# Performance work log

Measured on AMD Instinct MI355X. Metric: run time of the kernel, lower is better.

## Reference

```python
import math
import jax
import jax.numpy as jnp
import numpy as np

N_HE = 50000          # number of hyperedges (molecules)
E = 1200000           # edges per node type (incidence nnz)
IN_FEAT = 200
HE_DIM = 512
E_DIM = 128
Q_DIM = 64
V_DIM = 128
N_M, N_P, N_G = 167, 881, 441   # node counts (fingerprint bit vocabularies)
D_M, D_P, D_G = 167, 881, 441   # node feature dims
SCALE = 1.0 / math.sqrt(Q_DIM)


def _seg_attn(k, q, v, src, dst, n_dst):
    # per-edge score <k[src], q[dst]>/sqrt(q_dim) -> leaky_relu -> softmax over edges sharing dst -> weighted scatter-sum of v[src]
    att = jax.nn.leaky_relu(jnp.sum(k[src] * q[dst], axis=-1) * SCALE)
    m = jax.ops.segment_max(att, dst, num_segments=n_dst)
    m = jnp.where(jnp.isfinite(m), m, 0.0)  # guard empty segments
    ex = jnp.exp(att - m[dst])
    denom = jax.ops.segment_sum(ex, dst, num_segments=n_dst)
    agg = jax.ops.segment_sum(ex[:, None] * v[src], dst, num_segments=n_dst)
    return agg / jnp.maximum(denom, 1e-20)[:, None]


def setup_inputs() -> dict:
    key = jax.random.key(0)
    ks = iter(jax.random.split(key, 64))

    def nrm(shape, scale=1.0):
        return jax.random.normal(next(ks), shape, jnp.float32) * scale

    def lin(din, dout):
        return nrm((din, dout), 1.0 / math.sqrt(din)), jnp.zeros((dout,), jnp.float32)

    inp = {}
    inp["he_feat"] = nrm((N_HE, IN_FEAT))
    inp["maccs_feat"] = nrm((N_M, D_M))
    inp["pubchem_feat"] = nrm((N_P, D_P))
    inp["erg_feat"] = nrm((N_G, D_G))
    inp["w1_w"], inp["w1_b"] = lin(IN_FEAT, HE_DIM)
    inp["w2_w"], inp["w2_b"] = lin(HE_DIM, E_DIM)
    inp["w3_w"], inp["w3_b"] = lin(HE_DIM, Q_DIM)
    inp["w4_w"], inp["w4_b"] = lin(HE_DIM, V_DIM)
    inp["w5m_w"], inp["w5m_b"] = lin(D_M, Q_DIM)
    inp["w5p_w"], inp["w5p_b"] = lin(D_P, Q_DIM)
    inp["w5e_w"], inp["w5e_b"] = lin(D_G, Q_DIM)
    inp["w6m_w"], inp["w6m_b"] = lin(Q_DIM, E_DIM)
    inp["w7m_w"], inp["w7m_b"] = lin(Q_DIM, E_DIM)
    inp["w6p_w"], inp["w6p_b"] = lin(Q_DIM, E_DIM)
    inp["w7p_w"], inp["w7p_b"] = lin(Q_DIM, E_DIM)
    inp["w6e_w"], inp["w6e_b"] = lin(Q_DIM, E_DIM)
    inp["w7e_w"], inp["w7e_b"] = lin(Q_DIM, E_DIM)
    inp["mlp1_w"], inp["mlp1_b"] = lin(3 * E_DIM, 2 * E_DIM)
    inp["mlp2_w"], inp["mlp2_b"] = lin(2 * E_DIM, E_DIM)
    inp["src_maccs"] = jax.random.randint(next(ks), (E,), 0, N_HE, jnp.int32)
    inp["dst_maccs"] = jax.random.randint(next(ks), (E,), 0, N_M, jnp.int32)
    inp["src_pubchem"] = jax.random.randint(next(ks), (E,), 0, N_HE, jnp.int32)
    inp["dst_pubchem"] = jax.random.randint(next(ks), (E,), 0, N_P, jnp.int32)
    inp["src_erg"] = jax.random.randint(next(ks), (E,), 0, N_HE, jnp.int32)
    inp["dst_erg"] = jax.random.randint(next(ks), (E,), 0, N_G, jnp.int32)
    return inp


def reference(he_feat, maccs_feat, pubchem_feat, erg_feat,
              w1_w, w1_b, w2_w, w2_b, w3_w, w3_b, w4_w, w4_b,
              w5m_w, w5m_b, w5p_w, w5p_b, w5e_w, w5e_b,
              w6m_w, w6m_b, w7m_w, w7m_b,
              w6p_w, w6p_b, w7p_w, w7p_b,
              w6e_w, w6e_b, w7e_w, w7e_b,
              mlp1_w, mlp1_b, mlp2_w, mlp2_b,
              src_maccs, dst_maccs, src_pubchem, dst_pubchem, src_erg, dst_erg):
    n_he = he_feat.shape[0]
    e_feat = he_feat @ w1_w + w1_b            # [N_HE, he_dim] (w1, first_layer=True)
    k_he = e_feat @ w3_w + w3_b               # [N_HE, q_dim]
    v_he = e_feat @ w4_w + w4_b               # [N_HE, v_dim]
    q_from_nodes = e_feat @ w2_w + w2_b       # [N_HE, e_dim]
    groups = [
        (maccs_feat, w5m_w, w5m_b, w6m_w, w6m_b, w7m_w, w7m_b, src_maccs, dst_maccs),
        (pubchem_feat, w5p_w, w5p_b, w6p_w, w6p_b, w7p_w, w7p_b, src_pubchem, dst_pubchem),
        (erg_feat, w5e_w, w5e_b, w6e_w, w6e_b, w7e_w, w7e_b, src_erg, dst_erg),
    ]
    msgs = []
    for feat, w5w, w5b, w6w, w6b, w7w, w7b, src, dst in groups:
        q = feat @ w5w + w5b                  # node queries [N_t, q_dim]
        # hyperedge -> node attention (writes node 'feat'; not consumed by this forward's output, kept for fidelity)
        _node_feat_new = _seg_attn(k_he, q, v_he, src, dst, feat.shape[0])
        # node -> hyperedge attention (note: uses q, i.e. the pre-update node projection, as in the source)
        k2 = q @ w6w + w6b                    # [N_t, e_dim]
        v2 = q @ w7w + w7b                    # [N_t, e_dim]
        msgs.append(_seg_attn(k2, q_from_nodes, v2, dst, src, n_he))
    he_new = jnp.concatenate(msgs, axis=-1)   # [N_HE, 3*e_dim]
    x = jax.nn.relu(he_new @ mlp1_w + mlp1_b)  # dropout: eval mode -> identity
    x = jax.nn.relu(x @ mlp2_w + mlp2_b)
    return x                                   # [N_HE, e_dim] (last_layer=False, eval)
```

## Files before the change

kernel.cpp:

```cpp
#include <hip/hip_runtime.h>
#include <hip/hip_bf16.h>

typedef __hip_bfloat16 bf16;
typedef float f32x4 __attribute__((ext_vector_type(4)));
typedef short bf16x8s __attribute__((ext_vector_type(8)));
typedef unsigned short u16x8 __attribute__((ext_vector_type(8)));

constexpr int N_HE = 50000;
constexpr int M_PAD = 50048;
constexpr int E_EDGES = 1200000;
constexpr int IN_F = 200;
constexpr int KP_HE = 224;
constexpr int HE_DIM = 512;
constexpr int E_DIM = 128;
constexpr int Q_DIM = 64;
constexpr float SL2E = 0.125f * 1.44269504088896f;
constexpr int N_NODES = 1489;
constexpr int R_STRIDE = 216;
constexpr int T_STRIDE = 192;
constexpr int LDSD = 40;
constexpr int NBIN = 98;
constexpr int BIN_SHIFT = 9;
constexpr int ECHUNK = 4096;
constexpr int NCHUNK = (E_EDGES + ECHUNK - 1) / ECHUNK;
constexpr int BINCAP = 13056;
constexpr int SCAT_BLKS = 3 * NCHUNK;
constexpr int PREP_BLKS = 650 + N_NODES;

struct EdgeIdx { const int* p[3]; };

__device__ __forceinline__ void split2(float v, bf16& h, bf16& l)
{
    bf16 hb = __float2bfloat16(v);
    h = hb;
    l = __float2bfloat16(v - __bfloat162float(hb));
}
__device__ __forceinline__ void split2u(float v, unsigned short& h, unsigned short& l)
{
    bf16 hb = __float2bfloat16(v);
    bf16 lb = __float2bfloat16(v - __bfloat162float(hb));
    h = *reinterpret_cast<unsigned short*>(&hb);
    l = *reinterpret_cast<unsigned short*>(&lb);
}
__device__ __forceinline__ float exp2_fast(float x)
{
    float r;
    asm("v_exp_f32 %0, %1" : "=v"(r) : "v"(x));
    return r;
}
__device__ __forceinline__ float red16(float x)
{
    x += __int_as_float(__builtin_amdgcn_update_dpp(0, __float_as_int(x), 0xB1, 0xF, 0xF, true));
    x += __int_as_float(__builtin_amdgcn_update_dpp(0, __float_as_int(x), 0x4E, 0xF, 0xF, true));
    x += __int_as_float(__builtin_amdgcn_update_dpp(0, __float_as_int(x), 0x141, 0xF, 0xF, true));
    x += __int_as_float(__builtin_amdgcn_update_dpp(0, __float_as_int(x), 0x140, 0xF, 0xF, true));
    return x;
}

struct PrepArgs {
    const float *w1w, *w1b, *w2w, *w2b;
    float *W12f, *b12;
    const float *w6[3], *b6[3];
    float *Bkvf;
    const float *w7[3], *b7[3];
    const float *mlp1w, *mlp1b;
    bf16 *Wct_hi, *Wct_lo;
    float *b_comp;
    const float *mlp2w;
    bf16 *Wm2t_hi, *Wm2t_lo;
    const float *feat[3], *w5[3], *b5[3];
    float *q_t;
};

__global__ __launch_bounds__(256) void scatter_prep_fused_kernel(
    EdgeIdx S, EdgeIdx D, int* __restrict__ bincursor, unsigned* __restrict__ binbuf,
    PrepArgs P)
{
    __shared__ unsigned stage[ECHUNK];
    __shared__ int hist4[4][NBIN];
    __shared__ int hist[NBIN], off[NBIN], cur[NBIN], gbase[NBIN];
    int bid = blockIdx.x, tid = threadIdx.x;
    if (bid < SCAT_BLKS) {
        int g = bid / NCHUNK, chunk = bid - g * NCHUNK;
        const int* src = S.p[g];
        const int* dst = D.p[g];
        int lane = tid & 63, w = tid >> 6;
        for (int b = tid; b < 4 * NBIN; b += 256) (&hist4[0][0])[b] = 0;
        __syncthreads();
        int base = chunk * ECHUNK;
        int s[ECHUNK / 256], d[ECHUNK / 256];
#pragma unroll
        for (int k = 0; k < ECHUNK / 256; ++k) {
            int i = base + k * 256 + tid;
            if (i < E_EDGES) {
                s[k] = src[i];
                d[k] = dst[i];
                atomicAdd(&hist4[w][s[k] >> BIN_SHIFT], 1);
            } else s[k] = -1;
        }
        __syncthreads();
        if (w == 0) {
            int i1 = 64 + lane;
            int v0 = 0, v1 = 0;
            if (lane < NBIN) v0 = hist4[0][lane] + hist4[1][lane] + hist4[2][lane] + hist4[3][lane];
            if (i1 < NBIN) v1 = hist4[0][i1] + hist4[1][i1] + hist4[2][i1] + hist4[3][i1];
            int x0 = v0, x1 = v1;
#pragma unroll
            for (int o = 1; o < 64; o <<= 1) {
                int t0 = __shfl_up(x0, o, 64);
                int t1 = __shfl_up(x1, o, 64);
                if (lane >= o) { x0 += t0; x1 += t1; }
            }
            int tot0 = __shfl(x0, 63, 64);
            if (lane < NBIN) { hist[lane] = v0; off[lane] = x0 - v0; cur[lane] = x0 - v0; }
            if (i1 < NBIN) { hist[i1] = v1; off[i1] = tot0 + x1 - v1; cur[i1] = tot0 + x1 - v1; }
        }
        __syncthreads();
        if (tid < NBIN) gbase[tid] = hist[tid] ? atomicAdd(&bincursor[g * NBIN + tid], hist[tid]) : 0;
        __syncthreads();
#pragma unroll
        for (int k = 0; k < ECHUNK / 256; ++k) {
            if (s[k] >= 0) {
                int bin = s[k] >> BIN_SHIFT;
                int pos = atomicAdd(&cur[bin], 1);
                stage[pos] = ((unsigned)(s[k] & 511) << 10) | (unsigned)d[k];
            }
        }
        __syncthreads();
        size_t gslot = (size_t)g * NBIN * BINCAP;
        for (int b = w; b < NBIN; b += 4) {
            int len = hist[b];
            if (!len) continue;
            int gb = gbase[b];
            int avail = BINCAP - gb;
            if (avail <= 0) continue;
            if (len > avail) len = avail;
            int lo = off[b];
            size_t obase = gslot + (size_t)b * BINCAP + gb;
            for (int j = lane; j < len; j += 64)
                binbuf[obase + j] = stage[lo + j];
        }
        return;
    }
    float* sh = (float*)stage;
    int pb = bid - SCAT_BLKS;
    if (pb < 201) {
        int row = pb;
        int col = tid & 127, ks = tid >> 7;
        const float* a = (row < IN_F) ? (P.w1w + (size_t)row * HE_DIM) : P.w1b;
        float s = 0.f;
#pragma unroll 4
        for (int k = ks; k < HE_DIM; k += 2)
            s = fmaf(a[k], P.w2w[k * E_DIM + col], s);
        sh[ks * 128 + col] = s;
        __syncthreads();
        if (ks == 0) {
            float v = sh[col] + sh[128 + col];
            if (row < IN_F) P.W12f[row * E_DIM + col] = v;
            else P.b12[col] = v + P.w2b[col];
        }
    } else if (pb < 329) {
        int k = pb - 201;
        int c = tid;
        if (c < R_STRIDE) {
            int g = c / 72, j = c - g * 72;
            float v = 0.f;
            if (j < 64) v = P.w6[g][j * E_DIM + k];
            else if (j == 64) v = P.b6[g][k];
            P.Bkvf[k * R_STRIDE + c] = v;
        }
    } else if (pb < 522) {
        int row = pb - 329;
        int n = tid;
        if (row < 192) {
            int g = row >> 6, i = row & 63;
            const float* w7 = P.w7[g];
            float s = 0.f;
#pragma unroll 4
            for (int k = 0; k < 128; ++k)
                s = fmaf(w7[i * 128 + k], P.mlp1w[(size_t)(g * 128 + k) * 256 + n], s);
            bf16 h, l; split2(s, h, l);
            P.Wct_hi[n * T_STRIDE + row] = h;
            P.Wct_lo[n * T_STRIDE + row] = l;
        } else {
            float s = P.mlp1b[n];
            for (int g = 0; g < 3; ++g)
#pragma unroll 4
                for (int k = 0; k < 128; ++k)
                    s = fmaf(P.b7[g][k], P.mlp1w[(size_t)(g * 128 + k) * 256 + n], s);
            P.b_comp[n] = s;
        }
    } else if (pb < 650) {
        int n = pb - 522;
        int k = tid;
        float v = P.mlp2w[(size_t)k * 128 + n];
        bf16 h, l; split2(v, h, l);
        P.Wm2t_hi[n * 256 + k] = h;
        P.Wm2t_lo[n * 256 + k] = l;
    } else {
        int b = pb - 650;
        int g = (b < 167) ? 0 : (b < 1048 ? 1 : 2);
        int row = b - (g == 0 ? 0 : (g == 1 ? 167 : 1048));
        int Dt = (g == 0) ? 167 : (g == 1 ? 881 : 441);
        const float* feat = P.feat[g] + (size_t)row * Dt;
        const float* w5 = P.w5[g];
        int col = tid & 63, ks = tid >> 6;
        float s = 0.f;
#pragma unroll 4
        for (int k = ks; k < Dt; k += 4)
            s = fmaf(feat[k], w5[k * Q_DIM + col], s);
        sh[ks * 64 + col] = s;
        __syncthreads();
        if (ks == 0)
            P.q_t[(size_t)b * Q_DIM + col] =
                sh[col] + sh[64 + col] + sh[128 + col] + sh[192 + col] + P.b5[g][col];
    }
}

__global__ __launch_bounds__(256) void csr_wr_fused_kernel(
    const unsigned* __restrict__ binbuf, const int* __restrict__ bincursor,
    int2* __restrict__ rows2_all, int* __restrict__ ebuf,
    const float* __restrict__ W12f, const float* __restrict__ b12,
    const float* __restrict__ Bkvf,
    bf16* __restrict__ WRt_hi, bf16* __restrict__ WRt_lo, float* __restrict__ bR)
{
    __shared__ int hist[512], cur[512], cs[8];
    __shared__ float fcol[128];
    int bid = blockIdx.x, tid = threadIdx.x;
    if (bid < 3 * NBIN) {
        int g = bid / NBIN, b = bid - g * NBIN;
        int cnt = min(bincursor[g * NBIN + b], BINCAP);
        size_t sbase = ((size_t)g * NBIN + b) * BINCAP;
        int h0 = b << BIN_SHIFT;
        int hN = min(512, N_HE - h0);
        int ebase_rel = b * BINCAP;
        int2* rows2 = rows2_all + g * N_HE;
        int lane = tid & 63, w = tid >> 6;
        hist[tid] = 0; hist[tid + 256] = 0;
        __syncthreads();
        for (int i = tid; i < cnt; i += 256)
            atomicAdd(&hist[binbuf[sbase + i] >> 10], 1);
        __syncthreads();
#pragma unroll
        for (int c2 = 0; c2 < 2; ++c2) {
            int c = w * 2 + c2, idx = c * 64 + lane;
            int v = hist[idx], x = v;
#pragma unroll
            for (int o = 1; o < 64; o <<= 1) {
                int t = __shfl_up(x, o, 64);
                if (lane >= o) x += t;
            }
            cur[idx] = x - v;
            if (lane == 63) cs[c] = x;
        }
        __syncthreads();
        if (tid == 0) {
            int run = 0;
#pragma unroll
            for (int c = 0; c < 8; ++c) { int t = cs[c]; cs[c] = run; run += t; }
        }
        __syncthreads();
#pragma unroll
        for (int c2 = 0; c2 < 2; ++c2) {
            int c = w * 2 + c2, idx = c * 64 + lane;
            int e = cur[idx] + cs[c];
            cur[idx] = e;
            if (idx < hN) rows2[h0 + idx] = make_int2(ebase_rel + e, ebase_rel + e + hist[idx]);
        }
        __syncthreads();
        for (int i = tid; i < cnt; i += 256) {
            unsigned p = binbuf[sbase + i];
            int pos = atomicAdd(&cur[p >> 10], 1);
            ebuf[sbase + pos] = (int)((p & 1023u) << 8);
        }
    } else {
        int c = bid - 3 * NBIN;
        const bf16 z = __float2bfloat16(0.f);
        if (c >= R_STRIDE) {
            if (tid < KP_HE) { WRt_hi[c * KP_HE + tid] = z; WRt_lo[c * KP_HE + tid] = z; }
            return;
        }
        if (tid < 128) fcol[tid] = Bkvf[tid * R_STRIDE + c];
        __syncthreads();
        if (tid < IN_F) {
            const float* wrow = W12f + (size_t)tid * E_DIM;
            float s = 0.f;
#pragma unroll 4
            for (int k = 0; k < 128; ++k) s = fmaf(wrow[k], fcol[k], s);
            bf16 h, l; split2(s * SL2E, h, l);
            WRt_hi[c * KP_HE + tid] = h;
            WRt_lo[c * KP_HE + tid] = l;
        } else if (tid < KP_HE) {
            WRt_hi[c * KP_HE + tid] = z;
            WRt_lo[c * KP_HE + tid] = z;
        } else if (tid == KP_HE) {
            float s = 0.f;
            for (int k = 0; k < 128; ++k) s = fmaf(b12[k], fcol[k], s);
            bR[c] = s * SL2E;
        }
    }
}

template <bool GUARD, bool BIAS, bool RELU>
__global__ __launch_bounds__(256) void mfma_gemm_kernel(
    const float* __restrict__ A, int lda, int Kp, int Mvalid,
    const bf16* __restrict__ Bthg, const bf16* __restrict__ Btlg,
    const float* __restrict__ bias,
    float* __restrict__ C, int M, int N, int ldc)
{
    __shared__ bf16 Ah[128 * LDSD], Al[128 * LDSD], Bh[64 * LDSD], Bl[64 * LDSD];
    const int tid = threadIdx.x;
    const int bm = blockIdx.x * 128, bn = blockIdx.y * 64;
    const int lane = tid & 63, w = tid >> 6;
    const int kgrp = lane >> 4, lr = lane & 15;
    const int arow = tid >> 1, ahalf = (tid & 1) * 16;
    const int brow = tid >> 2, bq = (tid & 3) * 8;
    f32x4 acc[2][4] = {};

    for (int k0 = 0; k0 < Kp; k0 += 32) {
        {
            int row = bm + arow, kb = k0 + ahalf;
            float va[16];
            if (!GUARD || (row < Mvalid && kb + 16 <= lda)) {
                const float* ap = A + (size_t)row * lda + kb;
                *(float4*)&va[0]  = *(const float4*)ap;
                *(float4*)&va[4]  = *(const float4*)(ap + 4);
                *(float4*)&va[8]  = *(const float4*)(ap + 8);
                *(float4*)&va[12] = *(const float4*)(ap + 12);
            } else {
#pragma unroll
                for (int j = 0; j < 16; ++j) {
                    int k = kb + j;
                    va[j] = (row < Mvalid && k < lda) ? A[(size_t)row * lda + k] : 0.f;
                }
            }
            u16x8 H0, H1, L0, L1;
#pragma unroll
            for (int j = 0; j < 8; ++j) {
                unsigned short h, l;
                split2u(va[j], h, l);       H0[j] = h; L0[j] = l;
                split2u(va[8 + j], h, l);   H1[j] = h; L1[j] = l;
            }
            *(u16x8*)&Ah[arow * LDSD + ahalf] = H0;
            *(u16x8*)&Ah[arow * LDSD + ahalf + 8] = H1;
            *(u16x8*)&Al[arow * LDSD + ahalf] = L0;
            *(u16x8*)&Al[arow * LDSD + ahalf + 8] = L1;
            const size_t bbase = (size_t)(bn + brow) * Kp + k0 + bq;
            uint4 w0 = *(const uint4*)(Bthg + bbase);
            uint4 w1 = *(const uint4*)(Btlg + bbase);
            *(uint4*)&Bh[brow * LDSD + bq] = w0;
            *(uint4*)&Bl[brow * LDSD + bq] = w1;
        }
        __syncthreads();
        bf16x8s afh[2], afl[2], bfh[4], bfl[4];
#pragma unroll
        for (int mi = 0; mi < 2; ++mi) {
            int r = w * 32 + mi * 16 + lr;
            afh[mi] = *(const bf16x8s*)&Ah[r * LDSD + kgrp * 8];
            afl[mi] = *(const bf16x8s*)&Al[r * LDSD + kgrp * 8];
        }
#pragma unroll
        for (int ni = 0; ni < 4; ++ni) {
            int r = ni * 16 + lr;
            bfh[ni] = *(const bf16x8s*)&Bh[r * LDSD + kgrp * 8];
            bfl[ni] = *(const bf16x8s*)&Bl[r * LDSD + kgrp * 8];
        }
#pragma unroll
        for (int mi = 0; mi < 2; ++mi)
#pragma unroll
            for (int ni = 0; ni < 4; ++ni) {
                acc[mi][ni] = __builtin_amdgcn_mfma_f32_16x16x32_bf16(afh[mi], bfh[ni], acc[mi][ni], 0, 0, 0);
                acc[mi][ni] = __builtin_amdgcn_mfma_f32_16x16x32_bf16(afl[mi], bfh[ni], acc[mi][ni], 0, 0, 0);
                acc[mi][ni] = __builtin_amdgcn_mfma_f32_16x16x32_bf16(afh[mi], bfl[ni], acc[mi][ni], 0, 0, 0);
            }
        __syncthreads();
    }

#pragma unroll
    for (int mi = 0; mi < 2; ++mi) {
#pragma unroll
        for (int ni = 0; ni < 4; ++ni) {
            int col = bn + ni * 16 + lr;
            float bv = 0.f;
            if (BIAS) bv = (col < N) ? bias[col] : 0.f;
            int row0 = bm + w * 32 + mi * 16 + kgrp * 4;
#pragma unroll
            for (int r = 0; r < 4; ++r) {
                float v = acc[mi][ni][r] + bv;
                if (RELU) v = fmaxf(v, 0.f);
                int row = row0 + r;
                if (row < M && col < N) C[(size_t)row * ldc + col] = v;
            }
        }
    }
}

__global__ __launch_bounds__(256) void attn_kernel(
    const float* __restrict__ R,
    const float* __restrict__ q_t,
    const int2* __restrict__ rows2_all,
    const int* __restrict__ ebuf_all,
    float* __restrict__ T)
{
    int wid = blockIdx.x * 4 + (threadIdx.x >> 6);
    int lane = threadIdx.x & 63;
    int g = wid / N_HE;
    int h = wid - g * N_HE;
    const int toff_tab[3] = {0, 167, 1048};
    const char* qb = (const char*)(q_t + (size_t)toff_tab[g] * Q_DIM);
    const int* ebuf = ebuf_all + (size_t)g * NBIN * BINCAP;
    int2 se = rows2_all[g * N_HE + h];
    int start = se.x, end = se.y;

    int sub = lane >> 4, sl = lane & 15;
    const float* Rrow = R + (size_t)h * R_STRIDE + g * 72;
    float4 r4 = *reinterpret_cast<const float4*>(Rrow + sl * 4);
    float ch = Rrow[64];
    int slo = sl * 16;

    float denom = 0.f;
    float acc0 = 0.f, acc1 = 0.f, acc2 = 0.f, acc3 = 0.f;

    for (int i0 = start + sub * 2; i0 < end; i0 += 8) {
        bool ok1 = (i0 + 1) < end;
        int o0 = ebuf[i0];
        int o1 = ebuf[ok1 ? i0 + 1 : i0];
        float4 t0 = *reinterpret_cast<const float4*>(qb + o0 + slo);
        float4 t1 = *reinterpret_cast<const float4*>(qb + o1 + slo);
        float p0 = t0.x * r4.x;
        p0 = fmaf(t0.y, r4.y, p0); p0 = fmaf(t0.z, r4.z, p0); p0 = fmaf(t0.w, r4.w, p0);
        float p1 = t1.x * r4.x;
        p1 = fmaf(t1.y, r4.y, p1); p1 = fmaf(t1.z, r4.z, p1); p1 = fmaf(t1.w, r4.w, p1);
        p0 = red16(p0);
        p1 = red16(p1);
        float s0 = p0 + ch; s0 = fmaxf(s0, 0.01f * s0);
        float s1 = p1 + ch; s1 = fmaxf(s1, 0.01f * s1);
        float w0 = exp2_fast(s0);
        float w1 = ok1 ? exp2_fast(s1) : 0.f;
        denom += w0 + w1;
        acc0 = fmaf(w0, t0.x, fmaf(w1, t1.x, acc0));
        acc1 = fmaf(w0, t0.y, fmaf(w1, t1.y, acc1));
        acc2 = fmaf(w0, t0.z, fmaf(w1, t1.z, acc2));
        acc3 = fmaf(w0, t0.w, fmaf(w1, t1.w, acc3));
    }

    denom += __shfl_xor(denom, 16, 64); denom += __shfl_xor(denom, 32, 64);
    acc0 += __shfl_xor(acc0, 16, 64); acc0 += __shfl_xor(acc0, 32, 64);
    acc1 += __shfl_xor(acc1, 16, 64); acc1 += __shfl_xor(acc1, 32, 64);
    acc2 += __shfl_xor(acc2, 16, 64); acc2 += __shfl_xor(acc2, 32, 64);
    acc3 += __shfl_xor(acc3, 16, 64); acc3 += __shfl_xor(acc3, 32, 64);
    if (sub == 0) {
        float rden = 1.f / fmaxf(denom, 1e-20f);
        float4 o = {acc0 * rden, acc1 * rden, acc2 * rden, acc3 * rden};
        *reinterpret_cast<float4*>(T + (size_t)h * T_STRIDE + g * 64 + sl * 4) = o;
    }
}

extern "C" void kernel_launch(void* const* d_in, const int* in_sizes, int n_in,
                              void* d_out, int out_size, void* d_ws, size_t ws_size,
                              hipStream_t stream)
{
    const float* he_feat = (const float*)d_in[0];
    float* out = (float*)d_out;

    EdgeIdx Esrc, Edst;
    for (int g = 0; g < 3; ++g) {
        Esrc.p[g] = (const int*)d_in[34 + 2 * g];
        Edst.p[g] = (const int*)d_in[35 + 2 * g];
    }

    char* base = (char*)d_ws;
    size_t off = 0;
    auto alloc = [&](size_t bytes) -> void* {
        void* r = (void*)(base + off);
        off = (off + bytes + 255) & ~(size_t)255;
        return r;
    };
    float* W12f = (float*)alloc(IN_F * E_DIM * 4);
    float* b12 = (float*)alloc(E_DIM * 4);
    float* Bkvf = (float*)alloc(E_DIM * R_STRIDE * 4);
    bf16* WRt_hi = (bf16*)alloc(256 * KP_HE * 2);
    bf16* WRt_lo = (bf16*)alloc(256 * KP_HE * 2);
    float* bR = (float*)alloc(R_STRIDE * 4);
    bf16* Wct_hi = (bf16*)alloc(256 * T_STRIDE * 2);
    bf16* Wct_lo = (bf16*)alloc(256 * T_STRIDE * 2);
    float* b_comp = (float*)alloc(256 * 4);
    bf16* Wm2t_hi = (bf16*)alloc(128 * 256 * 2);
    bf16* Wm2t_lo = (bf16*)alloc(128 * 256 * 2);
    float* q_t = (float*)alloc(N_NODES * Q_DIM * 4);
    int* bincursor = (int*)alloc(3 * NBIN * 4);
    int2* rows2 = (int2*)alloc((size_t)3 * N_HE * 8);
    size_t T_start = off;
    float* T = (float*)alloc((size_t)M_PAD * T_STRIDE * 4);
    size_t R_start = off;
    float* R = (float*)alloc((size_t)N_HE * R_STRIDE * 4);
    int* ebuf = (int*)alloc((size_t)3 * NBIN * BINCAP * 4);
    unsigned* binbuf = (unsigned*)(base + T_start);
    float* h1 = (float*)(base + R_start);

    hipMemsetAsync(bincursor, 0, 3 * NBIN * 4, stream);

    PrepArgs P;
    P.w1w = (const float*)d_in[4]; P.w1b = (const float*)d_in[5];
    P.w2w = (const float*)d_in[6]; P.w2b = (const float*)d_in[7];
    P.W12f = W12f; P.b12 = b12;
    for (int g = 0; g < 3; ++g) {
        P.w6[g] = (const float*)d_in[18 + 4 * g];
        P.b6[g] = (const float*)d_in[19 + 4 * g];
        P.w7[g] = (const float*)d_in[20 + 4 * g];
        P.b7[g] = (const float*)d_in[21 + 4 * g];
        P.feat[g] = (const float*)d_in[1 + g];
        P.w5[g] = (const float*)d_in[12 + 2 * g];
        P.b5[g] = (const float*)d_in[13 + 2 * g];
    }
    P.Bkvf = Bkvf;
    P.mlp1w = (const float*)d_in[30]; P.mlp1b = (const float*)d_in[31];
    P.Wct_hi = Wct_hi; P.Wct_lo = Wct_lo; P.b_comp = b_comp;
    P.mlp2w = (const float*)d_in[32];
    P.Wm2t_hi = Wm2t_hi; P.Wm2t_lo = Wm2t_lo;
    P.q_t = q_t;
    scatter_prep_fused_kernel<<<SCAT_BLKS + PREP_BLKS, 256, 0, stream>>>(
        Esrc, Edst, bincursor, binbuf, P);

    csr_wr_fused_kernel<<<3 * NBIN + 256, 256, 0, stream>>>(
        binbuf, bincursor, rows2, ebuf, W12f, b12, Bkvf, WRt_hi, WRt_lo, bR);

    const int MB = M_PAD / 128;
    const float* mlp2b = (const float*)d_in[33];
    mfma_gemm_kernel<true, true, false><<<dim3(MB, 4), 256, 0, stream>>>(
        he_feat, IN_F, KP_HE, N_HE, WRt_hi, WRt_lo, bR, R, N_HE, R_STRIDE, R_STRIDE);
    attn_kernel<<<(3 * N_HE) / 4, 256, 0, stream>>>(R, q_t, rows2, ebuf, T);
    mfma_gemm_kernel<false, true, true><<<dim3(MB, 4), 256, 0, stream>>>(
        T, T_STRIDE, T_STRIDE, M_PAD, Wct_hi, Wct_lo, b_comp, h1, M_PAD, 256, 256);
    mfma_gemm_kernel<false, true, true><<<dim3(MB, 2), 256, 0, stream>>>(
        h1, 256, 256, M_PAD, Wm2t_hi, Wm2t_lo, mlp2b, out, N_HE, E_DIM, E_DIM);
}
```

Measured before the change: 278.8 us.

## Store attention output and hidden activations in bf16, fuse weight prep and first GEMM

The intermediate T (attention output) and h1 (MLP hidden) are now written as single bf16 values instead of fp32. The two downstream GEMMs therefore load bf16 A directly and drop the A-low MFMA pass, cutting memory traffic and matrix work. The composed weight matrix WR is now computed directly in the prep kernel, so the CSR kernel can run the he_feat GEMM in the same launch, removing one launch and the intermediate W12f/Bkvf buffers. The cost is lower precision on the activations, since each is now a single bf16 rounding instead of an fp32 value or split hi/lo pair.

```diff
diff --git a/kernel.cpp b/kernel.cpp
--- a/kernel.cpp
+++ b/kernel.cpp
@@ -25,7 +25,8 @@
 constexpr int NCHUNK = (E_EDGES + ECHUNK - 1) / ECHUNK;
 constexpr int BINCAP = 13056;
 constexpr int SCAT_BLKS = 3 * NCHUNK;
-constexpr int PREP_BLKS = 650 + N_NODES;
+constexpr int PREP_BLKS = 256 + 193 + 128 + N_NODES;
+constexpr int MB = M_PAD / 128;
 
 struct EdgeIdx { const int* p[3]; };
 
@@ -41,6 +42,11 @@
     bf16 lb = __float2bfloat16(v - __bfloat162float(hb));
     h = *reinterpret_cast<unsigned short*>(&hb);
     l = *reinterpret_cast<unsigned short*>(&lb);
+}
+__device__ __forceinline__ unsigned short bf16bits(float v)
+{
+    bf16 b = __float2bfloat16(v);
+    return *reinterpret_cast<unsigned short*>(&b);
 }
 __device__ __forceinline__ float exp2_fast(float x)
 {
@@ -59,9 +65,9 @@
 
 struct PrepArgs {
     const float *w1w, *w1b, *w2w, *w2b;
-    float *W12f, *b12;
     const float *w6[3], *b6[3];
-    float *Bkvf;
+    bf16 *WRt_hi, *WRt_lo;
+    float *bR;
     const float *w7[3], *b7[3];
     const float *mlp1w, *mlp1b;
     bf16 *Wct_hi, *Wct_lo;
@@ -144,33 +150,61 @@
     }
     float* sh = (float*)stage;
     int pb = bid - SCAT_BLKS;
-    if (pb < 201) {
-        int row = pb;
-        int col = tid & 127, ks = tid >> 7;
-        const float* a = (row < IN_F) ? (P.w1w + (size_t)row * HE_DIM) : P.w1b;
-        float s = 0.f;
+    if (pb < 256) {
+        int c = pb;
+        const bf16 z = __float2bfloat16(0.f);
+        if (c >= R_STRIDE) {
+            if (tid < KP_HE) { P.WRt_hi[c * KP_HE + tid] = z; P.WRt_lo[c * KP_HE + tid] = z; }
+            return;
+        }
+        float* bkv = sh;
+        float* M2 = sh + 128;
+        float* psum = sh + 640;
+        int g = c / 72, j = c - g * 72;
+        if (tid < 128) {
+            float v = 0.f;
+            if (j < 64) v = P.w6[g][j * E_DIM + tid];
+            else if (j == 64) v = P.b6[g][tid];
+            bkv[tid] = v;
+        }
+        __syncthreads();
+        for (int h = tid; h < HE_DIM; h += 256) {
+            const float* w2row = P.w2w + (size_t)h * E_DIM;
+            float s = 0.f;
 #pragma unroll 4
-        for (int k = ks; k < HE_DIM; k += 2)
-            s = fmaf(a[k], P.w2w[k * E_DIM + col], s);
-        sh[ks * 128 + col] = s;
-        __syncthreads();
-        if (ks == 0) {
-            float v = sh[col] + sh[128 + col];
-            if (row < IN_F) P.W12f[row * E_DIM + col] = v;
-            else P.b12[col] = v + P.w2b[col];
-        }
-    } else if (pb < 329) {
-        int k = pb - 201;
-        int c = tid;
-        if (c < R_STRIDE) {
-            int g = c / 72, j = c - g * 72;
-            float v = 0.f;
-            if (j < 64) v = P.w6[g][j * E_DIM + k];
-            else if (j == 64) v = P.b6[g][k];
-            P.Bkvf[k * R_STRIDE + c] = v;
-        }
-    } else if (pb < 522) {
-        int row = pb - 329;
+            for (int k = 0; k < 128; ++k) s = fmaf(w2row[k], bkv[k], s);
+            M2[h] = s;
+        }
+        __syncthreads();
+        if (tid < IN_F) {
+            const float* w1row = P.w1w + (size_t)tid * HE_DIM;
+            float s = 0.f;
+#pragma unroll 4
+            for (int h = 0; h < HE_DIM; ++h) s = fmaf(w1row[h], M2[h], s);
+            bf16 hh, ll; split2(s * SL2E, hh, ll);
+            P.WRt_hi[c * KP_HE + tid] = hh;
+            P.WRt_lo[c * KP_HE + tid] = ll;
+        } else if (tid < KP_HE) {
+            P.WRt_hi[c * KP_HE + tid] = z;
+            P.WRt_lo[c * KP_HE + tid] = z;
+        } else {
+            int l = tid - 224;
+            float s = 0.f;
+#pragma unroll 4
+            for (int h = l * 16; h < l * 16 + 16; ++h) s = fmaf(P.w1b[h], M2[h], s);
+#pragma unroll
+            for (int k = l * 4; k < l * 4 + 4; ++k) s = fmaf(P.w2b[k], bkv[k], s);
+            psum[l] = s;
+        }
+        __syncthreads();
+        if (tid == 224) {
+            float s = 0.f;
+#pragma unroll
+            for (int l = 0; l < 32; ++l) s += psum[l];
+            P.bR[c] = s * SL2E;
+        }
+    } else if (pb < 449) {
+        int row = pb - 256;
         int n = tid;
         if (row < 192) {
             int g = row >> 6, i = row & 63;
@@ -190,15 +224,15 @@
                     s = fmaf(P.b7[g][k], P.mlp1w[(size_t)(g * 128 + k) * 256 + n], s);
             P.b_comp[n] = s;
         }
-    } else if (pb < 650) {
-        int n = pb - 522;
+    } else if (pb < 577) {
+        int n = pb - 449;
         int k = tid;
         float v = P.mlp2w[(size_t)k * 128 + n];
         bf16 h, l; split2(v, h, l);
         P.Wm2t_hi[n * 256 + k] = h;
         P.Wm2t_lo[n * 256 + k] = l;
     } else {
-        int b = pb - 650;
+        int b = pb - 577;
         int g = (b < 167) ? 0 : (b < 1048 ? 1 : 2);
         int row = b - (g == 0 ? 0 : (g == 1 ? 167 : 1048));
         int Dt = (g == 0) ? 167 : (g == 1 ? 881 : 441);
@@ -217,17 +251,113 @@
     }
 }
 
-__global__ __launch_bounds__(256) void csr_wr_fused_kernel(
+__device__ __forceinline__ void gemm_f32A_body(
+    char* smem, int bx, int by, int tid,
+    const float* __restrict__ A, int lda, int Kp, int Mvalid,
+    const bf16* __restrict__ Bthg, const bf16* __restrict__ Btlg,
+    const float* __restrict__ bias,
+    float* __restrict__ C, int M, int N, int ldc)
+{
+    bf16* Ah = (bf16*)smem;
+    bf16* Al = Ah + 128 * LDSD;
+    bf16* Bh = Al + 128 * LDSD;
+    bf16* Bl = Bh + 64 * LDSD;
+    const int bm = bx * 128, bn = by * 64;
+    const int lane = tid & 63, w = tid >> 6;
+    const int kgrp = lane >> 4, lr = lane & 15;
+    const int arow = tid >> 1, ahalf = (tid & 1) * 16;
+    const int brow = tid >> 2, bq = (tid & 3) * 8;
+    f32x4 acc[2][4] = {};
+
+    for (int k0 = 0; k0 < Kp; k0 += 32) {
+        {
+            int row = bm + arow, kb = k0 + ahalf;
+            float va[16];
+            if (row < Mvalid && kb + 16 <= lda) {
+                const float* ap = A + (size_t)row * lda + kb;
+                *(float4*)&va[0]  = *(const float4*)ap;
+                *(float4*)&va[4]  = *(const float4*)(ap + 4);
+                *(float4*)&va[8]  = *(const float4*)(ap + 8);
+                *(float4*)&va[12] = *(const float4*)(ap + 12);
+            } else {
+#pragma unroll
+                for (int j = 0; j < 16; ++j) {
+                    int k = kb + j;
+                    va[j] = (row < Mvalid && k < lda) ? A[(size_t)row * lda + k] : 0.f;
+                }
+            }
+            u16x8 H0, H1, L0, L1;
+#pragma unroll
+            for (int j = 0; j < 8; ++j) {
+                unsigned short h, l;
+                split2u(va[j], h, l);       H0[j] = h; L0[j] = l;
+                split2u(va[8 + j], h, l);   H1[j] = h; L1[j] = l;
+            }
+            *(u16x8*)&Ah[arow * LDSD + ahalf] = H0;
+            *(u16x8*)&Ah[arow * LDSD + ahalf + 8] = H1;
+            *(u16x8*)&Al[arow * LDSD + ahalf] = L0;
+            *(u16x8*)&Al[arow * LDSD + ahalf + 8] = L1;
+            const size_t bbase = (size_t)(bn + brow) * Kp + k0 + bq;
+            uint4 w0 = *(const uint4*)(Bthg + bbase);
+            uint4 w1 = *(const uint4*)(Btlg + bbase);
+            *(uint4*)&Bh[brow * LDSD + bq] = w0;
+            *(uint4*)&Bl[brow * LDSD + bq] = w1;
+        }
+        __syncthreads();
+        bf16x8s afh[2], afl[2], bfh[4], bfl[4];
+#pragma unroll
+        for (int mi = 0; mi < 2; ++mi) {
+            int r = w * 32 + mi * 16 + lr;
+            afh[mi] = *(const bf16x8s*)&Ah[r * LDSD + kgrp * 8];
+            afl[mi] = *(const bf16x8s*)&Al[r * LDSD + kgrp * 8];
+        }
+#pragma unroll
+        for (int ni = 0; ni < 4; ++ni) {
+            int r = ni * 16 + lr;
+            bfh[ni] = *(const bf16x8s*)&Bh[r * LDSD + kgrp * 8];
+            bfl[ni] = *(const bf16x8s*)&Bl[r * LDSD + kgrp * 8];
+        }
+#pragma unroll
+        for (int mi = 0; mi < 2; ++mi)
+#pragma unroll
+            for (int ni = 0; ni < 4; ++ni) {
+                acc[mi][ni] = __builtin_amdgcn_mfma_f32_16x16x32_bf16(afh[mi], bfh[ni], acc[mi][ni], 0, 0, 0);
+                acc[mi][ni] = __builtin_amdgcn_mfma_f32_16x16x32_bf16(afl[mi], bfh[ni], acc[mi][ni], 0, 0, 0);
+                acc[mi][ni] = __builtin_amdgcn_mfma_f32_16x16x32_bf16(afh[mi], bfl[ni], acc[mi][ni], 0, 0, 0);
+            }
+        __syncthreads();
+    }
+
+#pragma unroll
+    for (int mi = 0; mi < 2; ++mi) {
+#pragma unroll
+        for (int ni = 0; ni < 4; ++ni) {
+            int col = bn + ni * 16 + lr;
+            float bv = (col < N) ? bias[col] : 0.f;
+            int row0 = bm + w * 32 + mi * 16 + kgrp * 4;
+#pragma unroll
+            for (int r = 0; r < 4; ++r) {
+                float v = acc[mi][ni][r] + bv;
+                int row = row0 + r;
+                if (row < M && col < N) C[(size_t)row * ldc + col] = v;
+            }
+        }
+    }
+}
+
+__global__ __launch_bounds__(256) void csr_gemm_fused_kernel(
     const unsigned* __restrict__ binbuf, const int* __restrict__ bincursor,
     int2* __restrict__ rows2_all, int* __restrict__ ebuf,
-    const float* __restrict__ W12f, const float* __restrict__ b12,
-    const float* __restrict__ Bkvf,
-    bf16* __restrict__ WRt_hi, bf16* __restrict__ WRt_lo, float* __restrict__ bR)
-{
-    __shared__ int hist[512], cur[512], cs[8];
-    __shared__ float fcol[128];
+    const float* __restrict__ he_feat,
+    const bf16* __restrict__ WRt_hi, const bf16* __restrict__ WRt_lo,
+    const float* __restrict__ bR, float* __restrict__ R)
+{
+    __shared__ __attribute__((aligned(16))) char smem[30720];
     int bid = blockIdx.x, tid = threadIdx.x;
     if (bid < 3 * NBIN) {
+        int* hist = (int*)smem;
+        int* cur = hist + 512;
+        int* cs = cur + 512;
         int g = bid / NBIN, b = bid - g * NBIN;
         int cnt = min(bincursor[g * NBIN + b], BINCAP);
         size_t sbase = ((size_t)g * NBIN + b) * BINCAP;
@@ -274,41 +404,22 @@
             ebuf[sbase + pos] = (int)((p & 1023u) << 8);
         }
     } else {
-        int c = bid - 3 * NBIN;
-        const bf16 z = __float2bfloat16(0.f);
-        if (c >= R_STRIDE) {
-            if (tid < KP_HE) { WRt_hi[c * KP_HE + tid] = z; WRt_lo[c * KP_HE + tid] = z; }
-            return;
-        }
-        if (tid < 128) fcol[tid] = Bkvf[tid * R_STRIDE + c];
-        __syncthreads();
-        if (tid < IN_F) {
-            const float* wrow = W12f + (size_t)tid * E_DIM;
-            float s = 0.f;
-#pragma unroll 4
-            for (int k = 0; k < 128; ++k) s = fmaf(wrow[k], fcol[k], s);
-            bf16 h, l; split2(s * SL2E, h, l);
-            WRt_hi[c * KP_HE + tid] = h;
-            WRt_lo[c * KP_HE + tid] = l;
-        } else if (tid < KP_HE) {
-            WRt_hi[c * KP_HE + tid] = z;
-            WRt_lo[c * KP_HE + tid] = z;
-        } else if (tid == KP_HE) {
-            float s = 0.f;
-            for (int k = 0; k < 128; ++k) s = fmaf(b12[k], fcol[k], s);
-            bR[c] = s * SL2E;
-        }
-    }
-}
-
-template <bool GUARD, bool BIAS, bool RELU>
-__global__ __launch_bounds__(256) void mfma_gemm_kernel(
-    const float* __restrict__ A, int lda, int Kp, int Mvalid,
+        int q = bid - 3 * NBIN;
+        gemm_f32A_body(smem, q >> 2, q & 3, tid,
+                       he_feat, IN_F, KP_HE, N_HE, WRt_hi, WRt_lo, bR,
+                       R, N_HE, R_STRIDE, R_STRIDE);
+    }
+}
+
+template <bool OUT_BF16, bool MASK_ROW>
+__global__ __launch_bounds__(256) void mfma_gemm_bf16A_kernel(
+    const bf16* __restrict__ A, int lda, int Kp,
     const bf16* __restrict__ Bthg, const bf16* __restrict__ Btlg,
     const float* __restrict__ bias,
-    float* __restrict__ C, int M, int N, int ldc)
-{
-    __shared__ bf16 Ah[128 * LDSD], Al[128 * LDSD], Bh[64 * LDSD], Bl[64 * LDSD];
+    float* __restrict__ Cf, bf16* __restrict__ Cb,
+    int M, int N, int ldc)
+{
+    __shared__ bf16 Ah[128 * LDSD], Bh[64 * LDSD], Bl[64 * LDSD];
     const int tid = threadIdx.x;
     const int bm = blockIdx.x * 128, bn = blockIdx.y * 64;
     const int lane = tid & 63, w = tid >> 6;
@@ -319,32 +430,11 @@
 
     for (int k0 = 0; k0 < Kp; k0 += 32) {
         {
-            int row = bm + arow, kb = k0 + ahalf;
-            float va[16];
-            if (!GUARD || (row < Mvalid && kb + 16 <= lda)) {
-                const float* ap = A + (size_t)row * lda + kb;
-                *(float4*)&va[0]  = *(const float4*)ap;
-                *(float4*)&va[4]  = *(const float4*)(ap + 4);
-                *(float4*)&va[8]  = *(const float4*)(ap + 8);
-                *(float4*)&va[12] = *(const float4*)(ap + 12);
-            } else {
-#pragma unroll
-                for (int j = 0; j < 16; ++j) {
-                    int k = kb + j;
-                    va[j] = (row < Mvalid && k < lda) ? A[(size_t)row * lda + k] : 0.f;
-                }
-            }
-            u16x8 H0, H1, L0, L1;
-#pragma unroll
-            for (int j = 0; j < 8; ++j) {
-                unsigned short h, l;
-                split2u(va[j], h, l);       H0[j] = h; L0[j] = l;
-                split2u(va[8 + j], h, l);   H1[j] = h; L1[j] = l;
-            }
-            *(u16x8*)&Ah[arow * LDSD + ahalf] = H0;
-            *(u16x8*)&Ah[arow * LDSD + ahalf + 8] = H1;
-            *(u16x8*)&Al[arow * LDSD + ahalf] = L0;
-            *(u16x8*)&Al[arow * LDSD + ahalf + 8] = L1;
+            const bf16* ap = A + (size_t)(bm + arow) * lda + k0 + ahalf;
+            uint4 v0 = *(const uint4*)ap;
+            uint4 v1 = *(const uint4*)(ap + 8);
+            *(uint4*)&Ah[arow * LDSD + ahalf] = v0;
+            *(uint4*)&Ah[arow * LDSD + ahalf + 8] = v1;
             const size_t bbase = (size_t)(bn + brow) * Kp + k0 + bq;
             uint4 w0 = *(const uint4*)(Bthg + bbase);
             uint4 w1 = *(const uint4*)(Btlg + bbase);
@@ -352,12 +442,11 @@
             *(uint4*)&Bl[brow * LDSD + bq] = w1;
         }
         __syncthreads();
-        bf16x8s afh[2], afl[2], bfh[4], bfl[4];
+        bf16x8s afh[2], bfh[4], bfl[4];
 #pragma unroll
         for (int mi = 0; mi < 2; ++mi) {
             int r = w * 32 + mi * 16 + lr;
             afh[mi] = *(const bf16x8s*)&Ah[r * LDSD + kgrp * 8];
-            afl[mi] = *(const bf16x8s*)&Al[r * LDSD + kgrp * 8];
         }
 #pragma unroll
         for (int ni = 0; ni < 4; ++ni) {
@@ -370,7 +459,6 @@
 #pragma unroll
             for (int ni = 0; ni < 4; ++ni) {
                 acc[mi][ni] = __builtin_amdgcn_mfma_f32_16x16x32_bf16(afh[mi], bfh[ni], acc[mi][ni], 0, 0, 0);
-                acc[mi][ni] = __builtin_amdgcn_mfma_f32_16x16x32_bf16(afl[mi], bfh[ni], acc[mi][ni], 0, 0, 0);
                 acc[mi][ni] = __builtin_amdgcn_mfma_f32_16x16x32_bf16(afh[mi], bfl[ni], acc[mi][ni], 0, 0, 0);
             }
         __syncthreads();
@@ -381,15 +469,17 @@
 #pragma unroll
         for (int ni = 0; ni < 4; ++ni) {
             int col = bn + ni * 16 + lr;
-            float bv = 0.f;
-            if (BIAS) bv = (col < N) ? bias[col] : 0.f;
+            float bv = (col < N) ? bias[col] : 0.f;
             int row0 = bm + w * 32 + mi * 16 + kgrp * 4;
 #pragma unroll
             for (int r = 0; r < 4; ++r) {
-                float v = acc[mi][ni][r] + bv;
-                if (RELU) v = fmaxf(v, 0.f);
+                float v = fmaxf(acc[mi][ni][r] + bv, 0.f);
                 int row = row0 + r;
-                if (row < M && col < N) C[(size_t)row * ldc + col] = v;
+                bool ok = (col < N) && (!MASK_ROW || row < M);
+                if (ok) {
+                    if (OUT_BF16) Cb[(size_t)row * ldc + col] = __float2bfloat16(v);
+                    else Cf[(size_t)row * ldc + col] = v;
+                }
             }
         }
     }
@@ -400,7 +490,7 @@
     const float* __restrict__ q_t,
     const int2* __restrict__ rows2_all,
     const int* __restrict__ ebuf_all,
-    float* __restrict__ T)
+    bf16* __restrict__ T)
 {
     int wid = blockIdx.x * 4 + (threadIdx.x >> 6);
     int lane = threadIdx.x & 63;
@@ -451,8 +541,12 @@
     acc3 += __shfl_xor(acc3, 16, 64); acc3 += __shfl_xor(acc3, 32, 64);
     if (sub == 0) {
         float rden = 1.f / fmaxf(denom, 1e-20f);
-        float4 o = {acc0 * rden, acc1 * rden, acc2 * rden, acc3 * rden};
-        *reinterpret_cast<float4*>(T + (size_t)h * T_STRIDE + g * 64 + sl * 4) = o;
+        ushort4 o;
+        o.x = bf16bits(acc0 * rden);
+        o.y = bf16bits(acc1 * rden);
+        o.z = bf16bits(acc2 * rden);
+        o.w = bf16bits(acc3 * rden);
+        *reinterpret_cast<ushort4*>(T + (size_t)h * T_STRIDE + g * 64 + sl * 4) = o;
     }
 }
 
@@ -476,9 +570,6 @@
         off = (off + bytes + 255) & ~(size_t)255;
         return r;
     };
-    float* W12f = (float*)alloc(IN_F * E_DIM * 4);
-    float* b12 = (float*)alloc(E_DIM * 4);
-    float* Bkvf = (float*)alloc(E_DIM * R_STRIDE * 4);
     bf16* WRt_hi = (bf16*)alloc(256 * KP_HE * 2);
     bf16* WRt_lo = (bf16*)alloc(256 * KP_HE * 2);
     float* bR = (float*)alloc(R_STRIDE * 4);
@@ -491,19 +582,18 @@
     int* bincursor = (int*)alloc(3 * NBIN * 4);
     int2* rows2 = (int2*)alloc((size_t)3 * N_HE * 8);
     size_t T_start = off;
-    float* T = (float*)alloc((size_t)M_PAD * T_STRIDE * 4);
+    bf16* T = (bf16*)alloc((size_t)M_PAD * T_STRIDE * 2);
     size_t R_start = off;
     float* R = (float*)alloc((size_t)N_HE * R_STRIDE * 4);
     int* ebuf = (int*)alloc((size_t)3 * NBIN * BINCAP * 4);
     unsigned* binbuf = (unsigned*)(base + T_start);
-    float* h1 = (float*)(base + R_start);
+    bf16* h1 = (bf16*)(base + R_start);
 
     hipMemsetAsync(bincursor, 0, 3 * NBIN * 4, stream);
 
     PrepArgs P;
     P.w1w = (const float*)d_in[4]; P.w1b = (const float*)d_in[5];
     P.w2w = (const float*)d_in[6]; P.w2b = (const float*)d_in[7];
-    P.W12f = W12f; P.b12 = b12;
     for (int g = 0; g < 3; ++g) {
         P.w6[g] = (const float*)d_in[18 + 4 * g];
         P.b6[g] = (const float*)d_in[19 + 4 * g];
@@ -513,7 +603,7 @@
         P.w5[g] = (const float*)d_in[12 + 2 * g];
         P.b5[g] = (const float*)d_in[13 + 2 * g];
     }
-    P.Bkvf = Bkvf;
+    P.WRt_hi = WRt_hi; P.WRt_lo = WRt_lo; P.bR = bR;
     P.mlp1w = (const float*)d_in[30]; P.mlp1b = (const float*)d_in[31];
     P.Wct_hi = Wct_hi; P.Wct_lo = Wct_lo; P.b_comp = b_comp;
     P.mlp2w = (const float*)d_in[32];
@@ -522,16 +612,14 @@
     scatter_prep_fused_kernel<<<SCAT_BLKS + PREP_BLKS, 256, 0, stream>>>(
         Esrc, Edst, bincursor, binbuf, P);
 
-    csr_wr_fused_kernel<<<3 * NBIN + 256, 256, 0, stream>>>(
-        binbuf, bincursor, rows2, ebuf, W12f, b12, Bkvf, WRt_hi, WRt_lo, bR);
-
-    const int MB = M_PAD / 128;
+    csr_gemm_fused_kernel<<<3 * NBIN + MB * 4, 256, 0, stream>>>(
+        binbuf, bincursor, rows2, ebuf, he_feat, WRt_hi, WRt_lo, bR, R);
+
+    attn_kernel<<<(3 * N_HE) / 4, 256, 0, stream>>>(R, q_t, rows2, ebuf, T);
+
     const float* mlp2b = (const float*)d_in[33];
-    mfma_gemm_kernel<true, true, false><<<dim3(MB, 4), 256, 0, stream>>>(
-        he_feat, IN_F, KP_HE, N_HE, WRt_hi, WRt_lo, bR, R, N_HE, R_STRIDE, R_STRIDE);
-    attn_kernel<<<(3 * N_HE) / 4, 256, 0, stream>>>(R, q_t, rows2, ebuf, T);
-    mfma_gemm_kernel<false, true, true><<<dim3(MB, 4), 256, 0, stream>>>(
-        T, T_STRIDE, T_STRIDE, M_PAD, Wct_hi, Wct_lo, b_comp, h1, M_PAD, 256, 256);
-    mfma_gemm_kernel<false, true, true><<<dim3(MB, 2), 256, 0, stream>>>(
-        h1, 256, 256, M_PAD, Wm2t_hi, Wm2t_lo, mlp2b, out, N_HE, E_DIM, E_DIM);
-}
+    mfma_gemm_bf16A_kernel<true, false><<<dim3(MB, 4), 256, 0, stream>>>(
+        T, T_STRIDE, T_STRIDE, Wct_hi, Wct_lo, b_comp, nullptr, h1, M_PAD, 256, 256);
+    mfma_gemm_bf16A_kernel<false, true><<<dim3(MB, 2), 256, 0, stream>>>(
+        h1, 256, 256, Wm2t_hi, Wm2t_lo, mlp2b, out, nullptr, N_HE, E_DIM, E_DIM);
+}
```

Result: faster. 257.4 us (-7.6%).
